# Optimization experiments

Hardware: AMD Instinct MI355X
Metric: run time of the kernel (lower is better)

The kernel has to match this reference:

```python
import jax, jax.numpy as jnp
import numpy as np

LEAK = 0.2  # LeakyReLU alpha

def setup_inputs() -> dict:
    key = jax.random.key(0)
    k1, k2, k3, k4 = jax.random.split(key, 4)
    B, N, D, H = 4, 1024, 64, 64
    qs = jax.random.normal(k1, (B, N, D), dtype=jnp.float32)
    ks = jax.random.normal(k2, (B, N, D), dtype=jnp.float32)
    vs = jax.random.normal(k3, (B, N, D), dtype=jnp.float32)
    W = jax.random.normal(k4, (3 * D, H), dtype=jnp.float32) * 0.05  # Dense kernel on concat(q,k,q-k)
    b = jnp.zeros((H,), dtype=jnp.float32)
    a = jnp.ones((H,), dtype=jnp.float32)
    return {"qs": qs, "ks": ks, "vs": vs, "W": W, "b": b, "a": a}

def reference(qs, ks, vs, W, b, a):
    D = qs.shape[-1]
    norm = 1.0 / jnp.sqrt(jnp.asarray(D, dtype=qs.dtype))
    # Dense on concat(q, k, q-k) splits as q@(Wq+Wd) + k@(Wk-Wd) + b,
    # avoiding the O(N^2 * 3D) concat tensor (same math as TF concat->Dense).
    Wq, Wk, Wd = W[:D], W[D:2 * D], W[2 * D:]
    hq = qs @ (Wq + Wd)            # [B, N, H]  query-side term
    hk = ks @ (Wk - Wd)            # [B, N, H]  key-side term
    h = hq[:, :, None, :] + hk[:, None, :, :] + b   # [B, N, N, H]
    h = jnp.where(h > 0, h, LEAK * h)               # LeakyReLU(0.2)
    scores = jnp.einsum('bijh,h->bij', h, a) * norm # [B, N, N]
    att = jax.nn.softmax(scores, axis=-1)
    return jnp.matmul(att, vs)                      # [B, N, D]
```

## Files before the change

kernel.cpp:

```cpp
#include <hip/hip_runtime.h>
#include <math.h>

#define LOG2E 1.4426950408889634f
typedef __attribute__((ext_vector_type(2))) _Float16 h2v;
typedef __attribute__((ext_vector_type(8))) _Float16 f16x8;
typedef __attribute__((ext_vector_type(4))) float f32x4;

static __device__ __forceinline__ unsigned pkrtz_u32(float lo, float hi) {
  auto p = __builtin_amdgcn_cvt_pkrtz(lo, hi);
  unsigned u; __builtin_memcpy(&u, &p, 4); return u;
}
static __device__ __forceinline__ h2v habs2(h2v x) {
  unsigned u; __builtin_memcpy(&u, &x, 4);
  u &= 0x7FFF7FFFu;
  h2v r; __builtin_memcpy(&r, &u, 4); return r;
}
static __device__ __forceinline__ h2v u2h(unsigned u) {
  h2v r; __builtin_memcpy(&r, &u, 4); return r;
}


__global__ __launch_bounds__(256) void prep_kernel(
    const float* __restrict__ qs, const float* __restrict__ ks,
    const float* __restrict__ vs,
    const float* __restrict__ W, const float* __restrict__ bias,
    const float* __restrict__ a,
    unsigned* __restrict__ hq2, uint4* __restrict__ khT4,
    float* __restrict__ Dj, unsigned* __restrict__ abd2,
    uint4* __restrict__ vfrag) {
  __shared__ __align__(16) float wcomb[64][68];
  __shared__ __align__(16) float xin[64][68];
  const int blk = blockIdx.x;
  const int t = threadIdx.x;

  if (blk >= 128) {
    const int unit = blk - 128;
    const int b = unit >> 5, kstep = unit & 31;
    const int lane = t & 63, ntile = t >> 6;
    const int j0 = kstep * 32 + (lane >> 4) * 8;
    const int d = ntile * 16 + (lane & 15);
    const float* vb = vs + b * 1024 * 64;
    unsigned pr[4];
#pragma unroll
    for (int i = 0; i < 4; ++i)
      pr[i] = pkrtz_u32(vb[(j0 + 2 * i) * 64 + d], vb[(j0 + 2 * i + 1) * 64 + d]);
    vfrag[((b * 32 + kstep) * 4 + ntile) * 64 + lane] =
        make_uint4(pr[0], pr[1], pr[2], pr[3]);
    return;
  }

  const bool qpart = blk < 64;
  const int r0 = (qpart ? blk : blk - 64) * 64;
  const float* src = qpart ? qs : ks;
  if (blk == 0 && t < 32)
    abd2[t] = pkrtz_u32(0.05f * a[2 * t], 0.05f * a[2 * t + 1]);
  for (int rep = 0; rep < 16; ++rep) {
    int e = rep * 256 + t;
    int row = e >> 6, col = e & 63;
    float wd = W[(128 + row) * 64 + col];
    float wm = qpart ? (W[row * 64 + col] + wd)
                     : (W[(64 + row) * 64 + col] - wd);
    wcomb[row][col] = wm;
    xin[row][col] = src[(r0 + row) * 64 + col];
  }
  __syncthreads();
  const int r = t >> 2;
  const int h0 = (t & 3) << 4;
  float acc[16];
#pragma unroll
  for (int k = 0; k < 16; ++k) acc[k] = 0.f;
#pragma unroll 8
  for (int d = 0; d < 64; ++d) {
    float xv = xin[r][d];
#pragma unroll
    for (int c = 0; c < 4; ++c) {
      float4 w4 = *(const float4*)&wcomb[d][h0 + (c << 2)];
      acc[c * 4 + 0] = fmaf(xv, w4.x, acc[c * 4 + 0]);
      acc[c * 4 + 1] = fmaf(xv, w4.y, acc[c * 4 + 1]);
      acc[c * 4 + 2] = fmaf(xv, w4.z, acc[c * 4 + 2]);
      acc[c * 4 + 3] = fmaf(xv, w4.w, acc[c * 4 + 3]);
    }
  }
  int grow = r0 + r;
  if (qpart) {
    unsigned pr[8];
#pragma unroll
    for (int i = 0; i < 8; ++i) pr[i] = pkrtz_u32(acc[2 * i], acc[2 * i + 1]);
    uint4* dst = (uint4*)&hq2[grow * 32 + (t & 3) * 8];
    dst[0] = make_uint4(pr[0], pr[1], pr[2], pr[3]);
    dst[1] = make_uint4(pr[4], pr[5], pr[6], pr[7]);
  } else {
    int bidx = grow >> 10;
    int j = grow & 1023;
    float val[16];
    float part = 0.f;
#pragma unroll
    for (int k = 0; k < 16; ++k) {
      val[k] = acc[k] + bias[h0 + k];
      part += a[h0 + k] * val[k];
    }
    part += __shfl_xor(part, 1);
    part += __shfl_xor(part, 2);
    if ((t & 3) == 0) Dj[bidx * 1024 + j] = 0.075f * part;
    unsigned pr[8];
#pragma unroll
    for (int i = 0; i < 8; ++i) pr[i] = pkrtz_u32(val[2 * i], val[2 * i + 1]);
    const int h4a = (t & 3) * 2;
    khT4[(bidx * 8 + h4a) * 1024 + j]     = make_uint4(pr[0], pr[1], pr[2], pr[3]);
    khT4[(bidx * 8 + h4a + 1) * 1024 + j] = make_uint4(pr[4], pr[5], pr[6], pr[7]);
  }
}

__global__ __launch_bounds__(256) void attn13_kernel(
    const uint4* __restrict__ vfrag,
    const unsigned* __restrict__ hq2, const uint4* __restrict__ khT4,
    const float* __restrict__ Dj, const unsigned* __restrict__ abd2,
    float* __restrict__ out) {
  __shared__ __align__(16) unsigned p2u[4 * 520];
  __shared__ __align__(16) float ob[16 * 64];
  __shared__ __align__(16) unsigned q2lds[4 * 32];
  __shared__ __align__(16) unsigned ab2lds[32];
  __shared__ float redm[4][4];
  __shared__ float redl[4][4];

  const int t = threadIdx.x;
  const int lane = t & 63;
  const int w = t >> 6;
  const int b = blockIdx.y;
  const int rowbase = blockIdx.x * 4;
  const int growbase = b * 1024 + rowbase;

  const uint4* kh_b = khT4 + (size_t)b * 8 * 1024;
  const uint4* vf_b = vfrag + (size_t)b * 32 * 4 * 64;

  if (t < 128) q2lds[t] = hq2[growbase * 32 + t];
  if (t >= 128 && t < 160) ab2lds[t - 128] = abd2[t - 128];
  __syncthreads();

  const int jloc = w * 256 + lane * 4;
  float4 d4 = *(const float4*)(Dj + b * 1024 + jloc);

  float s[4][4];
#pragma unroll
  for (int r = 0; r < 4; ++r)
#pragma unroll
    for (int c = 0; c < 4; ++c) s[r][c] = 0.f;

  uint4 kc0 = kh_b[jloc], kc1 = kh_b[jloc + 1], kc2 = kh_b[jloc + 2],
        kc3 = kh_b[jloc + 3];
#pragma unroll 1
  for (int it = 0; it < 8; ++it) {
    const int nx = (it < 7) ? it + 1 : it;
    uint4 kn0 = kh_b[nx * 1024 + jloc];
    uint4 kn1 = kh_b[nx * 1024 + jloc + 1];
    uint4 kn2 = kh_b[nx * 1024 + jloc + 2];
    uint4 kn3 = kh_b[nx * 1024 + jloc + 3];
    uint4 abq = *(const uint4*)&ab2lds[it * 4];
    const unsigned abu[4] = {abq.x, abq.y, abq.z, abq.w};
    const unsigned kcu[4][4] = {{kc0.x, kc0.y, kc0.z, kc0.w},
                                {kc1.x, kc1.y, kc1.z, kc1.w},
                                {kc2.x, kc2.y, kc2.z, kc2.w},
                                {kc3.x, kc3.y, kc3.z, kc3.w}};
#pragma unroll
    for (int r = 0; r < 4; ++r) {
      uint4 qq = *(const uint4*)&q2lds[r * 32 + it * 4];
      const unsigned qu[4] = {qq.x, qq.y, qq.z, qq.w};
#pragma unroll
      for (int u = 0; u < 4; ++u) {
        h2v qh = u2h(qu[u]);
        h2v a2 = u2h(abu[u]);
#pragma unroll
        for (int c = 0; c < 4; ++c) {
          h2v x = habs2(qh + u2h(kcu[c][u]));
          s[r][c] = __builtin_amdgcn_fdot2(a2, x, s[r][c], false);
        }
      }
    }
    kc0 = kn0; kc1 = kn1; kc2 = kn2; kc3 = kn3;
  }
#pragma unroll
  for (int r = 0; r < 4; ++r) {
    s[r][0] += d4.x; s[r][1] += d4.y; s[r][2] += d4.z; s[r][3] += d4.w;
  }

#pragma unroll
  for (int r = 0; r < 4; ++r) {
    float m = fmaxf(fmaxf(s[r][0], s[r][1]), fmaxf(s[r][2], s[r][3]));
#pragma unroll
    for (int off = 32; off >= 1; off >>= 1) m = fmaxf(m, __shfl_xor(m, off));
    if (lane == 0) redm[r][w] = m;
  }
  __syncthreads();
  float mx[4];
#pragma unroll
  for (int r = 0; r < 4; ++r) {
    float4 rm = *(const float4*)&redm[r][0];
    mx[r] = fmaxf(fmaxf(rm.x, rm.y), fmaxf(rm.z, rm.w));
  }
#pragma unroll
  for (int r = 0; r < 4; ++r) {
    float p0 = __builtin_amdgcn_exp2f((s[r][0] - mx[r]) * LOG2E);
    float p1 = __builtin_amdgcn_exp2f((s[r][1] - mx[r]) * LOG2E);
    float p2 = __builtin_amdgcn_exp2f((s[r][2] - mx[r]) * LOG2E);
    float p3 = __builtin_amdgcn_exp2f((s[r][3] - mx[r]) * LOG2E);
    *(uint2*)&p2u[r * 520 + (jloc >> 1)] =
        make_uint2(pkrtz_u32(p0, p1), pkrtz_u32(p2, p3));
    float ps = (p0 + p1) + (p2 + p3);
#pragma unroll
    for (int off = 32; off >= 1; off >>= 1) ps += __shfl_xor(ps, off);
    if (lane == 0) redl[r][w] = ps;
  }
  __syncthreads();

  f32x4 acc[4];
#pragma unroll
  for (int nt = 0; nt < 4; ++nt) acc[nt] = (f32x4){0.f, 0.f, 0.f, 0.f};
  const int arow = (lane & 3) * 520;
  const int kgr = (lane >> 4) * 8;
#pragma unroll 2
  for (int ks = 0; ks < 8; ++ks) {
    const int j0 = w * 256 + ks * 32;
    uint4 au = *(const uint4*)&p2u[arow + ((j0 + kgr) >> 1)];
    f16x8 af; __builtin_memcpy(&af, &au, 16);
    const int gks = j0 >> 5;
#pragma unroll
    for (int nt = 0; nt < 4; ++nt) {
      uint4 bu = vf_b[(gks * 4 + nt) * 64 + lane];
      f16x8 bf; __builtin_memcpy(&bf, &bu, 16);
      acc[nt] = __builtin_amdgcn_mfma_f32_16x16x32_f16(af, bf, acc[nt], 0, 0, 0);
    }
  }

  if (lane < 16) {
#pragma unroll
    for (int nt = 0; nt < 4; ++nt)
#pragma unroll
      for (int rg = 0; rg < 4; ++rg)
        ob[(w * 4 + rg) * 64 + nt * 16 + lane] = acc[nt][rg];
  }
  __syncthreads();
  {
    int r = t >> 6, d = t & 63;
    float ax = 0.f;
#pragma unroll
    for (int wv = 0; wv < 4; ++wv) ax += ob[(wv * 4 + r) * 64 + d];
    float4 rl = *(const float4*)&redl[r][0];
    float inv = 1.f / ((rl.x + rl.y) + (rl.z + rl.w));
    out[(growbase + r) * 64 + d] = ax * inv;
  }
}

extern "C" void kernel_launch(void* const* d_in, const int* in_sizes, int n_in,
                              void* d_out, int out_size, void* d_ws, size_t ws_size,
                              hipStream_t stream) {
  const float* qs = (const float*)d_in[0];
  const float* ks = (const float*)d_in[1];
  const float* vs = (const float*)d_in[2];
  const float* W  = (const float*)d_in[3];
  const float* bi = (const float*)d_in[4];
  const float* a  = (const float*)d_in[5];
  float* out = (float*)d_out;
  unsigned* hq2   = (unsigned*)d_ws;
  uint4*    khT4  = (uint4*)((char*)d_ws + 524288);
  float*    Dj    = (float*)((char*)d_ws + 1048576);
  unsigned* abd2  = (unsigned*)((char*)d_ws + 1064960);
  uint4*    vfrag = (uint4*)((char*)d_ws + 1065216);
  prep_kernel<<<256, 256, 0, stream>>>(qs, ks, vs, W, bi, a, hq2, khT4, Dj,
                                       abd2, vfrag);
  attn13_kernel<<<dim3(256, 4), 256, 0, stream>>>(vfrag, hq2, khT4, Dj, abd2, out);
}
```

Before: 36.64 us.

## Process eight query rows per 512-thread block with two keys per thread

Each attention block now handles eight query rows with eight waves, and each thread covers two keys across all eight rows instead of four keys across four rows. The key-side hk tiles and value fragments are now reused across twice as many query rows per block, which halves how often they are fetched from global memory per row. The cost is a larger LDS footprint, a bigger per-thread score array, eight-way cross-wave reductions, and only 512 blocks in the grid. The MFMA accumulation uses 8 of the 16 A rows instead of 4.

```diff
diff --git a/kernel.cpp b/kernel.cpp
--- a/kernel.cpp
+++ b/kernel.cpp
@@ -111,101 +111,90 @@
   }
 }
 
-__global__ __launch_bounds__(256) void attn13_kernel(
+__global__ __launch_bounds__(512) void attn14_kernel(
     const uint4* __restrict__ vfrag,
     const unsigned* __restrict__ hq2, const uint4* __restrict__ khT4,
     const float* __restrict__ Dj, const unsigned* __restrict__ abd2,
     float* __restrict__ out) {
-  __shared__ __align__(16) unsigned p2u[4 * 520];
-  __shared__ __align__(16) float ob[16 * 64];
-  __shared__ __align__(16) unsigned q2lds[4 * 32];
+  __shared__ __align__(16) unsigned p2u[8 * 520];
+  __shared__ __align__(16) float ob[64 * 64];
+  __shared__ __align__(16) unsigned q2lds[8 * 32];
   __shared__ __align__(16) unsigned ab2lds[32];
-  __shared__ float redm[4][4];
-  __shared__ float redl[4][4];
+  __shared__ float redm[8][8];
+  __shared__ float redl[8][8];
 
   const int t = threadIdx.x;
   const int lane = t & 63;
   const int w = t >> 6;
   const int b = blockIdx.y;
-  const int rowbase = blockIdx.x * 4;
+  const int rowbase = blockIdx.x * 8;
   const int growbase = b * 1024 + rowbase;
 
   const uint4* kh_b = khT4 + (size_t)b * 8 * 1024;
   const uint4* vf_b = vfrag + (size_t)b * 32 * 4 * 64;
 
-  if (t < 128) q2lds[t] = hq2[growbase * 32 + t];
-  if (t >= 128 && t < 160) ab2lds[t - 128] = abd2[t - 128];
-  __syncthreads();
-
-  const int jloc = w * 256 + lane * 4;
-  float4 d4 = *(const float4*)(Dj + b * 1024 + jloc);
-
-  float s[4][4];
-#pragma unroll
-  for (int r = 0; r < 4; ++r)
-#pragma unroll
-    for (int c = 0; c < 4; ++c) s[r][c] = 0.f;
-
-  uint4 kc0 = kh_b[jloc], kc1 = kh_b[jloc + 1], kc2 = kh_b[jloc + 2],
-        kc3 = kh_b[jloc + 3];
+  if (t < 256) q2lds[t] = hq2[growbase * 32 + t];
+  if (t >= 256 && t < 288) ab2lds[t - 256] = abd2[t - 256];
+  __syncthreads();
+
+  const int jloc = w * 128 + lane * 2;
+  float2 d2 = *(const float2*)(Dj + b * 1024 + jloc);
+
+  float s[8][2];
+#pragma unroll
+  for (int r = 0; r < 8; ++r) { s[r][0] = 0.f; s[r][1] = 0.f; }
+
+  uint4 kc0 = kh_b[jloc], kc1 = kh_b[jloc + 1];
 #pragma unroll 1
   for (int it = 0; it < 8; ++it) {
     const int nx = (it < 7) ? it + 1 : it;
     uint4 kn0 = kh_b[nx * 1024 + jloc];
     uint4 kn1 = kh_b[nx * 1024 + jloc + 1];
-    uint4 kn2 = kh_b[nx * 1024 + jloc + 2];
-    uint4 kn3 = kh_b[nx * 1024 + jloc + 3];
     uint4 abq = *(const uint4*)&ab2lds[it * 4];
     const unsigned abu[4] = {abq.x, abq.y, abq.z, abq.w};
-    const unsigned kcu[4][4] = {{kc0.x, kc0.y, kc0.z, kc0.w},
-                                {kc1.x, kc1.y, kc1.z, kc1.w},
-                                {kc2.x, kc2.y, kc2.z, kc2.w},
-                                {kc3.x, kc3.y, kc3.z, kc3.w}};
-#pragma unroll
-    for (int r = 0; r < 4; ++r) {
+    const unsigned kcu[2][4] = {{kc0.x, kc0.y, kc0.z, kc0.w},
+                                {kc1.x, kc1.y, kc1.z, kc1.w}};
+#pragma unroll
+    for (int r = 0; r < 8; ++r) {
       uint4 qq = *(const uint4*)&q2lds[r * 32 + it * 4];
       const unsigned qu[4] = {qq.x, qq.y, qq.z, qq.w};
 #pragma unroll
       for (int u = 0; u < 4; ++u) {
         h2v qh = u2h(qu[u]);
         h2v a2 = u2h(abu[u]);
-#pragma unroll
-        for (int c = 0; c < 4; ++c) {
-          h2v x = habs2(qh + u2h(kcu[c][u]));
-          s[r][c] = __builtin_amdgcn_fdot2(a2, x, s[r][c], false);
-        }
+        h2v x0 = habs2(qh + u2h(kcu[0][u]));
+        s[r][0] = __builtin_amdgcn_fdot2(a2, x0, s[r][0], false);
+        h2v x1 = habs2(qh + u2h(kcu[1][u]));
+        s[r][1] = __builtin_amdgcn_fdot2(a2, x1, s[r][1], false);
       }
     }
-    kc0 = kn0; kc1 = kn1; kc2 = kn2; kc3 = kn3;
-  }
-#pragma unroll
-  for (int r = 0; r < 4; ++r) {
-    s[r][0] += d4.x; s[r][1] += d4.y; s[r][2] += d4.z; s[r][3] += d4.w;
-  }
-
-#pragma unroll
-  for (int r = 0; r < 4; ++r) {
-    float m = fmaxf(fmaxf(s[r][0], s[r][1]), fmaxf(s[r][2], s[r][3]));
+    kc0 = kn0; kc1 = kn1;
+  }
+#pragma unroll
+  for (int r = 0; r < 8; ++r) { s[r][0] += d2.x; s[r][1] += d2.y; }
+
+#pragma unroll
+  for (int r = 0; r < 8; ++r) {
+    float m = fmaxf(s[r][0], s[r][1]);
 #pragma unroll
     for (int off = 32; off >= 1; off >>= 1) m = fmaxf(m, __shfl_xor(m, off));
     if (lane == 0) redm[r][w] = m;
   }
   __syncthreads();
-  float mx[4];
-#pragma unroll
-  for (int r = 0; r < 4; ++r) {
-    float4 rm = *(const float4*)&redm[r][0];
-    mx[r] = fmaxf(fmaxf(rm.x, rm.y), fmaxf(rm.z, rm.w));
-  }
-#pragma unroll
-  for (int r = 0; r < 4; ++r) {
+  float mx[8];
+#pragma unroll
+  for (int r = 0; r < 8; ++r) {
+    float4 a0 = *(const float4*)&redm[r][0];
+    float4 a1 = *(const float4*)&redm[r][4];
+    mx[r] = fmaxf(fmaxf(fmaxf(a0.x, a0.y), fmaxf(a0.z, a0.w)),
+                  fmaxf(fmaxf(a1.x, a1.y), fmaxf(a1.z, a1.w)));
+  }
+#pragma unroll
+  for (int r = 0; r < 8; ++r) {
     float p0 = __builtin_amdgcn_exp2f((s[r][0] - mx[r]) * LOG2E);
     float p1 = __builtin_amdgcn_exp2f((s[r][1] - mx[r]) * LOG2E);
-    float p2 = __builtin_amdgcn_exp2f((s[r][2] - mx[r]) * LOG2E);
-    float p3 = __builtin_amdgcn_exp2f((s[r][3] - mx[r]) * LOG2E);
-    *(uint2*)&p2u[r * 520 + (jloc >> 1)] =
-        make_uint2(pkrtz_u32(p0, p1), pkrtz_u32(p2, p3));
-    float ps = (p0 + p1) + (p2 + p3);
+    p2u[r * 520 + (jloc >> 1)] = pkrtz_u32(p0, p1);
+    float ps = p0 + p1;
 #pragma unroll
     for (int off = 32; off >= 1; off >>= 1) ps += __shfl_xor(ps, off);
     if (lane == 0) redl[r][w] = ps;
@@ -215,11 +204,11 @@
   f32x4 acc[4];
 #pragma unroll
   for (int nt = 0; nt < 4; ++nt) acc[nt] = (f32x4){0.f, 0.f, 0.f, 0.f};
-  const int arow = (lane & 3) * 520;
+  const int arow = (lane & 7) * 520;
   const int kgr = (lane >> 4) * 8;
 #pragma unroll 2
-  for (int ks = 0; ks < 8; ++ks) {
-    const int j0 = w * 256 + ks * 32;
+  for (int ks = 0; ks < 4; ++ks) {
+    const int j0 = w * 128 + ks * 32;
     uint4 au = *(const uint4*)&p2u[arow + ((j0 + kgr) >> 1)];
     f16x8 af; __builtin_memcpy(&af, &au, 16);
     const int gks = j0 >> 5;
@@ -231,22 +220,24 @@
     }
   }
 
-  if (lane < 16) {
+  if (lane < 32) {
+    const int rbase = (lane >> 4) * 4;
 #pragma unroll
     for (int nt = 0; nt < 4; ++nt)
 #pragma unroll
       for (int rg = 0; rg < 4; ++rg)
-        ob[(w * 4 + rg) * 64 + nt * 16 + lane] = acc[nt][rg];
+        ob[(w * 8 + rbase + rg) * 64 + nt * 16 + (lane & 15)] = acc[nt][rg];
   }
   __syncthreads();
   {
     int r = t >> 6, d = t & 63;
     float ax = 0.f;
 #pragma unroll
-    for (int wv = 0; wv < 4; ++wv) ax += ob[(wv * 4 + r) * 64 + d];
-    float4 rl = *(const float4*)&redl[r][0];
-    float inv = 1.f / ((rl.x + rl.y) + (rl.z + rl.w));
-    out[(growbase + r) * 64 + d] = ax * inv;
+    for (int wv = 0; wv < 8; ++wv) ax += ob[(wv * 8 + r) * 64 + d];
+    float4 l0 = *(const float4*)&redl[r][0];
+    float4 l1 = *(const float4*)&redl[r][4];
+    float lt = ((l0.x + l0.y) + (l0.z + l0.w)) + ((l1.x + l1.y) + (l1.z + l1.w));
+    out[(growbase + r) * 64 + d] = ax / lt;
   }
 }
 
@@ -267,5 +258,5 @@
   uint4*    vfrag = (uint4*)((char*)d_ws + 1065216);
   prep_kernel<<<256, 256, 0, stream>>>(qs, ks, vs, W, bi, a, hq2, khT4, Dj,
                                        abd2, vfrag);
-  attn13_kernel<<<dim3(256, 4), 256, 0, stream>>>(vfrag, hq2, khT4, Dj, abd2, out);
-}
+  attn14_kernel<<<dim3(128, 4), 512, 0, stream>>>(vfrag, hq2, khT4, Dj, abd2, out);
+}
```

Result: no change. 36.30 us (-0.9%).
